# Performance work log

Measured on AMD Instinct MI355X. Metric: run time of the kernel, lower is better.

## Reference

```python
import jax, jax.numpy as jnp
import numpy as np

B, T, C = 4, 4096, 128

def setup_inputs() -> dict:
    key = jax.random.key(0)
    k1, k2, k3, k4 = jax.random.split(key, 4)
    x = jax.random.normal(k1, (B, T, C), dtype=jnp.float32)
    s = 1.0 / np.sqrt(C)
    Wq = jax.random.normal(k2, (C, C), dtype=jnp.float32) * s
    Wk = jax.random.normal(k3, (C, C), dtype=jnp.float32) * s
    Wv = jax.random.normal(k4, (C, C), dtype=jnp.float32) * s
    return {"x": x, "Wq": Wq, "Wk": Wk, "Wv": Wv}

def reference(x, Wq, Wk, Wv):
    # nn.Linear(bias=False): y = x @ W.T
    q = jnp.einsum('btc,dc->btd', x, Wq)
    k = jnp.einsum('btc,dc->btd', x, Wk)
    v = jnp.einsum('btc,dc->btd', x, Wv)
    scale = 1.0 / jnp.sqrt(jnp.asarray(x.shape[-1], x.dtype))
    att = jnp.einsum('btd,bsd->bts', q, k) * scale  # [B,T,T]
    causal = jnp.tril(jnp.ones((x.shape[1], x.shape[1]), dtype=bool))
    att = jnp.where(causal[None, :, :], att, -jnp.inf)
    w = jax.nn.softmax(att, axis=-1)
    # dropout p=0.0 -> identity
    out = jnp.einsum('bts,bsd->btd', w, v)
    return out
```

## Files before the change

kernel.cpp:

```cpp
#include <hip/hip_runtime.h>
#include <hip/hip_bf16.h>
#include <math.h>

#define T_SEQ 4096
#define C_DIM 128
#define B_SZ  4

typedef __attribute__((ext_vector_type(8))) short short8;
typedef __attribute__((ext_vector_type(4))) short short4v;
typedef __attribute__((ext_vector_type(4))) float f32x4;

__device__ __forceinline__ short f2bf(float f) {
    union { float fv; unsigned u; } v; v.fv = f;
    unsigned r = v.u + 0x7fff + ((v.u >> 16) & 1);
    return (short)(r >> 16);
}

__device__ __forceinline__ unsigned pk_bf16(float a, float b) {
    union { __hip_bfloat162 h2; unsigned u; } c;
    c.h2 = __float22bfloat162_rn(make_float2(a, b));
    return c.u;
}

__device__ __forceinline__ short8 load_f32x8_bf16(const float* p) {
    const float4* q = (const float4*)p;
    float4 a = q[0], b = q[1];
    short8 r;
    r[0] = f2bf(a.x); r[1] = f2bf(a.y); r[2] = f2bf(a.z); r[3] = f2bf(a.w);
    r[4] = f2bf(b.x); r[5] = f2bf(b.y); r[6] = f2bf(b.z); r[7] = f2bf(b.w);
    return r;
}

__device__ __forceinline__ void async_cp16(const short* g, short* l) {
    __builtin_amdgcn_global_load_lds(
        (const __attribute__((address_space(1))) unsigned int*)g,
        (__attribute__((address_space(3))) unsigned int*)l, 16, 0, 0);
}

__global__ __launch_bounds__(512) void qkv_proj(
    const float* __restrict__ x, const float* __restrict__ Wq,
    const float* __restrict__ Wk, const float* __restrict__ Wv,
    short* __restrict__ Q, short* __restrict__ Kf, short* __restrict__ Vf)
{
    __shared__ short8 Wl[2048];

    const int tid  = threadIdx.x;
    const int lane = tid & 63;
    const int ln15 = lane & 15;
    const int quad = lane >> 4;
    const int mat  = blockIdx.x >> 6;
    const int rt   = (blockIdx.x & 63) * 8 + (tid >> 6);
    const int m0   = rt * 32;

    const float* W = (mat == 0) ? Wq : (mat == 1) ? Wk : Wv;

    for (int i = tid; i < 2048; i += 512) {
        int n = i >> 4, kc = i & 15;
        short8 v = load_f32x8_bf16(W + n * C_DIM + kc * 8);
        Wl[((n >> 4) * 4 + (kc >> 2)) * 64 + (kc & 3) * 16 + (n & 15)] = v;
    }

    short8 afr[2][4];
#pragma unroll
    for (int ms = 0; ms < 2; ++ms) {
        const float* xrow = x + (size_t)(m0 + ms * 16 + ln15) * C_DIM + quad * 8;
#pragma unroll
        for (int ks = 0; ks < 4; ++ks)
            afr[ms][ks] = load_f32x8_bf16(xrow + ks * 32);
    }

    __syncthreads();

    const float scale = (mat == 0) ? (0.08838834764831845f * 1.4426950408889634f)
                                   : 1.0f;
    const int b  = m0 >> 12;
    const int tl = m0 & 4095;

#pragma unroll
    for (int nt = 0; nt < 8; ++nt) {
        f32x4 acc0 = {0.f, 0.f, 0.f, 0.f};
        f32x4 acc1 = {0.f, 0.f, 0.f, 0.f};
#pragma unroll
        for (int ks = 0; ks < 4; ++ks) {
            short8 bfr = Wl[(nt * 4 + ks) * 64 + lane];
            if (mat == 2) {
                acc0 = __builtin_amdgcn_mfma_f32_16x16x32_bf16(afr[0][ks], bfr, acc0, 0, 0, 0);
                acc1 = __builtin_amdgcn_mfma_f32_16x16x32_bf16(afr[1][ks], bfr, acc1, 0, 0, 0);
            } else {
                acc0 = __builtin_amdgcn_mfma_f32_16x16x32_bf16(bfr, afr[0][ks], acc0, 0, 0, 0);
                acc1 = __builtin_amdgcn_mfma_f32_16x16x32_bf16(bfr, afr[1][ks], acc1, 0, 0, 0);
            }
        }
        if (mat == 0) {
            short4v s0, s1;
#pragma unroll
            for (int r = 0; r < 4; ++r) { s0[r] = f2bf(acc0[r] * scale); s1[r] = f2bf(acc1[r] * scale); }
            *(short4v*)&Q[(size_t)(m0 + ln15) * C_DIM + nt * 16 + quad * 4]      = s0;
            *(short4v*)&Q[(size_t)(m0 + 16 + ln15) * C_DIM + nt * 16 + quad * 4] = s1;
        } else if (mat == 1) {
            const int t16 = tl >> 4;
            short4v s0, s1;
#pragma unroll
            for (int r = 0; r < 4; ++r) { s0[r] = f2bf(acc0[r]); s1[r] = f2bf(acc1[r]); }
            size_t base = (((size_t)(b * 256 + t16) * 4 + (nt >> 1)) << 9)
                        + (((nt & 1) * 2 + (quad >> 1)) * 128) + ln15 * 8 + (quad & 1) * 4;
            *(short4v*)&Kf[base]        = s0;
            *(short4v*)&Kf[base + 2048] = s1;
        } else {
            const int kvc = tl >> 5;
            short4v s0, s1;
#pragma unroll
            for (int r = 0; r < 4; ++r) { s0[r] = f2bf(acc0[r]); s1[r] = f2bf(acc1[r]); }
            short* vbase = Vf + (((size_t)(b * 128 + kvc) * 8 + nt) << 9);
            *(short4v*)&vbase[((quad >> 1) * 16 + ln15) * 8 + (quad & 1) * 4]       = s0;
            *(short4v*)&vbase[(((quad >> 1) + 2) * 16 + ln15) * 8 + (quad & 1) * 4] = s1;
        }
    }
}


#define ROUND_BODY(KC, VC, KN, VN, R)                                        \
  {                                                                          \
    const int kv0 = (R) << 6;                                                \
     \
    asm volatile("s_waitcnt vmcnt(0)" ::: "memory");                         \
    __builtin_amdgcn_sched_barrier(0);                                       \
    __builtin_amdgcn_s_barrier();                                            \
    __builtin_amdgcn_sched_barrier(0);                                       \
    if ((R) + 1 <= kmax) {                                                   \
      const short* gk = Kb + ((size_t)((R) + 1) << 13) + w * 1024;           \
      const short* gv = Vb + ((size_t)((R) + 1) << 13) + w * 1024;           \
      _Pragma("unroll")                                                      \
      for (int i = 0; i < 2; ++i) {                                          \
        async_cp16(gk + i * 512 + lane * 8, &KN[w * 1024 + i * 512]);        \
        async_cp16(gv + i * 512 + lane * 8, &VN[w * 1024 + i * 512]);        \
      }                                                                      \
    }                                                                        \
     \
    short8 kfr[4];                                                           \
    _Pragma("unroll")                                                        \
    for (int ks = 0; ks < 4; ++ks)                                           \
      kfr[ks] = *(const short8*)&KC[(wg * 4 + ks) * 512 + lane * 8];         \
    f32x4 St = {0.f, 0.f, 0.f, 0.f};                                         \
    _Pragma("unroll")                                                        \
    for (int ks = 0; ks < 4; ++ks)                                           \
      St = __builtin_amdgcn_mfma_f32_16x16x32_bf16(kfr[ks], qf[ks], St,      \
                                                   0, 0, 0);                 \
    if (kv0 + 64 > q0) {                                                     \
      const int qcol = q0 + ln15;                                            \
      _Pragma("unroll")                                                      \
      for (int rr = 0; rr < 4; ++rr)                                         \
        if (kv0 + wg * 16 + quad * 4 + rr > qcol) St[rr] = -INFINITY;        \
    }                                                                        \
    {                                                                        \
      float p0 = __builtin_amdgcn_exp2f(St[0] - 16.f);                       \
      float p1 = __builtin_amdgcn_exp2f(St[1] - 16.f);                       \
      float p2 = __builtin_amdgcn_exp2f(St[2] - 16.f);                       \
      float p3 = __builtin_amdgcn_exp2f(St[3] - 16.f);                       \
      l_i += (p0 + p1) + (p2 + p3);                                          \
      uint2 pk;                                                              \
      pk.x = pk_bf16(p0, p1);                                                \
      pk.y = pk_bf16(p2, p3);                                                \
      *(uint2*)&Plds[g][ln15 * 68 + wg * 16 + quad * 4] = pk;                \
    }                                                                        \
           \
    asm volatile("s_waitcnt lgkmcnt(0)" ::: "memory");                       \
    __builtin_amdgcn_sched_barrier(0);                                       \
    __builtin_amdgcn_s_barrier();                                            \
    __builtin_amdgcn_sched_barrier(0);                                       \
           \
    _Pragma("unroll")                                                        \
    for (int kc = 0; kc < 2; ++kc) {                                         \
      short8 vfr[2];                                                         \
      _Pragma("unroll")                                                      \
      for (int di = 0; di < 2; ++di)                                         \
        vfr[di] =                                                            \
            *(const short8*)&VC[(kc * 8 + wg * 2 + di) * 512 + lane * 8];    \
      short8 pf = *(const short8*)&Plds[g][ln15 * 68 + kc * 32 + quad * 8];  \
      _Pragma("unroll")                                                      \
      for (int di = 0; di < 2; ++di)                                         \
        acc[di] = __builtin_amdgcn_mfma_f32_16x16x32_bf16(                   \
            vfr[di], pf, acc[di], 0, 0, 0);                                  \
    }                                                                        \
  }

__global__ __launch_bounds__(512, 2) void flash_attn(
    const short* __restrict__ Q, const short* __restrict__ Kf,
    const short* __restrict__ Vf, float* __restrict__ out)
{
    __shared__ short Klds0[8192];
    __shared__ short Klds1[8192];
    __shared__ short Vlds0[8192];
    __shared__ short Vlds1[8192];
    __shared__ short Plds[2][1088];
    __shared__ float lsum[2][16];

    const int tid  = threadIdx.x;
    const int w    = tid >> 6;
    const int lane = tid & 63;
    const int ln15 = lane & 15;
    const int quad = lane >> 4;
    const int g    = w >> 2;
    const int wg   = w & 3;
    const int bid  = blockIdx.x;
    const int b    = bid & 3;
    const int jj   = bid >> 2;

    const short* Qb = Q  + (size_t)b * T_SEQ * C_DIM;
    const short* Kb = Kf + ((size_t)b << 19);
    const short* Vb = Vf + ((size_t)b << 19);
    float* outb = out + (size_t)b * T_SEQ * C_DIM;

    for (int half = 0; half < 2; ++half) {
        const int p    = half ? (127 - jj) : jj;
        const int q0   = p * 32 + g * 16;
        const int kmax = (p * 32 + 31) >> 6;

        short8 qf[4];
        {
            const short* qrow = Qb + (size_t)(q0 + ln15) * C_DIM + quad * 8;
#pragma unroll
            for (int ks = 0; ks < 4; ++ks)
                qf[ks] = *(const short8*)(qrow + ks * 32);
        }

        f32x4 acc[2];
#pragma unroll
        for (int di = 0; di < 2; ++di)
            acc[di] = (f32x4){0.f, 0.f, 0.f, 0.f};
        float l_i = 0.f;

        {
            const short* gk = Kb + w * 1024;
            const short* gv = Vb + w * 1024;
#pragma unroll
            for (int i = 0; i < 2; ++i) {
                async_cp16(gk + i * 512 + lane * 8, &Klds0[w * 1024 + i * 512]);
                async_cp16(gv + i * 512 + lane * 8, &Vlds0[w * 1024 + i * 512]);
            }
        }

        int r = 0;
        while (true) {
            ROUND_BODY(Klds0, Vlds0, Klds1, Vlds1, r);
            if (++r > kmax) break;
            ROUND_BODY(Klds1, Vlds1, Klds0, Vlds0, r);
            if (++r > kmax) break;
        }

        __syncthreads();
        if (tid < 32) ((float*)lsum)[tid] = 0.f;
        __syncthreads();
        atomicAdd(&lsum[g][ln15], l_i);
        __syncthreads();

        const float li = 1.0f / lsum[g][ln15];
        float* orow = outb + (size_t)(q0 + ln15) * C_DIM;
#pragma unroll
        for (int di = 0; di < 2; ++di) {
            float4 v = make_float4(acc[di][0] * li, acc[di][1] * li,
                                   acc[di][2] * li, acc[di][3] * li);
            *(float4*)&orow[(wg * 2 + di) * 16 + quad * 4] = v;
        }
        __syncthreads();
    }
}

extern "C" void kernel_launch(void* const* d_in, const int* in_sizes, int n_in,
                              void* d_out, int out_size, void* d_ws, size_t ws_size,
                              hipStream_t stream) {
    const float* x  = (const float*)d_in[0];
    const float* Wq = (const float*)d_in[1];
    const float* Wk = (const float*)d_in[2];
    const float* Wv = (const float*)d_in[3];
    float* out = (float*)d_out;

    const size_t elems = (size_t)B_SZ * T_SEQ * C_DIM;
    short* Q  = (short*)d_ws;
    short* Kf = Q  + elems;
    short* Vf = Kf + elems;

    hipLaunchKernelGGL(qkv_proj, dim3(192), dim3(512), 0, stream,
                       x, Wq, Wk, Wv, Q, Kf, Vf);
    hipLaunchKernelGGL(flash_attn, dim3(256), dim3(512), 0, stream,
                       Q, Kf, Vf, out);
}
```

Baseline: 131.4 us.

## Split KV across waves so P stays in registers, removing mid-round barrier

```diff
diff --git a/kernel.cpp b/kernel.cpp
--- a/kernel.cpp
+++ b/kernel.cpp
@@ -98,14 +98,30 @@
             *(short4v*)&Q[(size_t)(m0 + ln15) * C_DIM + nt * 16 + quad * 4]      = s0;
             *(short4v*)&Q[(size_t)(m0 + 16 + ln15) * C_DIM + nt * 16 + quad * 4] = s1;
         } else if (mat == 1) {
-            const int t16 = tl >> 4;
             short4v s0, s1;
 #pragma unroll
             for (int r = 0; r < 4; ++r) { s0[r] = f2bf(acc0[r]); s1[r] = f2bf(acc1[r]); }
-            size_t base = (((size_t)(b * 256 + t16) * 4 + (nt >> 1)) << 9)
-                        + (((nt & 1) * 2 + (quad >> 1)) * 128) + ln15 * 8 + (quad & 1) * 4;
-            *(short4v*)&Kf[base]        = s0;
-            *(short4v*)&Kf[base + 2048] = s1;
+            const int ks     = nt >> 1;
+            const int quad_k = (nt & 1) * 2 + (quad >> 1);
+            const int j0     = (quad & 1) * 4;
+            {
+                const int A0 = (tl >> 4) & 3;
+                const int rd = tl >> 6;
+                const int kt = (A0 >> 1) * 2 + ((ln15 >> 2) & 1);
+                const int ar = (((A0 & 1) << 1) | ((ln15 >> 3) & 1)) * 4 + (ln15 & 3);
+                size_t a = ((size_t)b << 19) + (size_t)rd * 8192
+                         + (kt * 4 + ks) * 512 + quad_k * 128 + ar * 8 + j0;
+                *(short4v*)&Kf[a] = s0;
+            }
+            {
+                const int A1 = ((tl >> 4) + 1) & 3;
+                const int rd = (tl + 16) >> 6;
+                const int kt = (A1 >> 1) * 2 + ((ln15 >> 2) & 1);
+                const int ar = (((A1 & 1) << 1) | ((ln15 >> 3) & 1)) * 4 + (ln15 & 3);
+                size_t a = ((size_t)b << 19) + (size_t)rd * 8192
+                         + (kt * 4 + ks) * 512 + quad_k * 128 + ar * 8 + j0;
+                *(short4v*)&Kf[a] = s1;
+            }
         } else {
             const int kvc = tl >> 5;
             short4v s0, s1;
@@ -128,63 +144,60 @@
     __builtin_amdgcn_s_barrier();                                            \
     __builtin_amdgcn_sched_barrier(0);                                       \
     if ((R) + 1 <= kmax) {                                                   \
-      const short* gk = Kb + ((size_t)((R) + 1) << 13) + w * 1024;           \
-      const short* gv = Vb + ((size_t)((R) + 1) << 13) + w * 1024;           \
+      const short* gk = Kb + (size_t)((R) + 1) * 8192 + w * 2048;            \
+      const short* gv = Vb + (size_t)((R) + 1) * 8192 + w * 2048;            \
       _Pragma("unroll")                                                      \
-      for (int i = 0; i < 2; ++i) {                                          \
-        async_cp16(gk + i * 512 + lane * 8, &KN[w * 1024 + i * 512]);        \
-        async_cp16(gv + i * 512 + lane * 8, &VN[w * 1024 + i * 512]);        \
+      for (int i = 0; i < 4; ++i) {                                          \
+        async_cp16(gk + i * 512 + lane * 8, &KN[w * 2048 + i * 512]);        \
+        async_cp16(gv + i * 512 + lane * 8, &VN[w * 2048 + i * 512]);        \
       }                                                                      \
     }                                                                        \
+              \
+    f32x4 St0 = {0.f, 0.f, 0.f, 0.f}, St1 = {0.f, 0.f, 0.f, 0.f};            \
+    _Pragma("unroll")                                                        \
+    for (int ks = 0; ks < 4; ++ks) {                                         \
+      short8 k0 = *(const short8*)&KC[((s2 + 0) * 4 + ks) * 512 + lane * 8]; \
+      short8 k1 = *(const short8*)&KC[((s2 + 1) * 4 + ks) * 512 + lane * 8]; \
+      St0 = __builtin_amdgcn_mfma_f32_16x16x32_bf16(k0, qf[ks], St0, 0,0,0); \
+      St1 = __builtin_amdgcn_mfma_f32_16x16x32_bf16(k1, qf[ks], St1, 0,0,0); \
+    }                                                                        \
+    \
+    if (kv0 + s * 32 + 31 > q0w) {                                           \
+      const int qcol = q0w + ln15;                                           \
+      const int kb   = kv0 + s * 32 + quad * 8;                              \
+      _Pragma("unroll")                                                      \
+      for (int rr = 0; rr < 4; ++rr) {                                       \
+        if (kb + rr > qcol)     St0[rr] = -INFINITY;                         \
+        if (kb + 4 + rr > qcol) St1[rr] = -INFINITY;                         \
+      }                                                                      \
+    }                                                                        \
      \
-    short8 kfr[4];                                                           \
+    union { unsigned u[4]; short8 s8; } pa;                                  \
+    {                                                                        \
+      float p0 = __builtin_amdgcn_exp2f(St0[0] - 16.f);                      \
+      float p1 = __builtin_amdgcn_exp2f(St0[1] - 16.f);                      \
+      float p2 = __builtin_amdgcn_exp2f(St0[2] - 16.f);                      \
+      float p3 = __builtin_amdgcn_exp2f(St0[3] - 16.f);                      \
+      float p4 = __builtin_amdgcn_exp2f(St1[0] - 16.f);                      \
+      float p5 = __builtin_amdgcn_exp2f(St1[1] - 16.f);                      \
+      float p6 = __builtin_amdgcn_exp2f(St1[2] - 16.f);                      \
+      float p7 = __builtin_amdgcn_exp2f(St1[3] - 16.f);                      \
+      l_i += ((p0 + p1) + (p2 + p3)) + ((p4 + p5) + (p6 + p7));              \
+      pa.u[0] = pk_bf16(p0, p1);                                             \
+      pa.u[1] = pk_bf16(p2, p3);                                             \
+      pa.u[2] = pk_bf16(p4, p5);                                             \
+      pa.u[3] = pk_bf16(p6, p7);                                             \
+    }                                                                        \
+                           \
     _Pragma("unroll")                                                        \
-    for (int ks = 0; ks < 4; ++ks)                                           \
-      kfr[ks] = *(const short8*)&KC[(wg * 4 + ks) * 512 + lane * 8];         \
-    f32x4 St = {0.f, 0.f, 0.f, 0.f};                                         \
-    _Pragma("unroll")                                                        \
-    for (int ks = 0; ks < 4; ++ks)                                           \
-      St = __builtin_amdgcn_mfma_f32_16x16x32_bf16(kfr[ks], qf[ks], St,      \
-                                                   0, 0, 0);                 \
-    if (kv0 + 64 > q0) {                                                     \
-      const int qcol = q0 + ln15;                                            \
-      _Pragma("unroll")                                                      \
-      for (int rr = 0; rr < 4; ++rr)                                         \
-        if (kv0 + wg * 16 + quad * 4 + rr > qcol) St[rr] = -INFINITY;        \
-    }                                                                        \
-    {                                                                        \
-      float p0 = __builtin_amdgcn_exp2f(St[0] - 16.f);                       \
-      float p1 = __builtin_amdgcn_exp2f(St[1] - 16.f);                       \
-      float p2 = __builtin_amdgcn_exp2f(St[2] - 16.f);                       \
-      float p3 = __builtin_amdgcn_exp2f(St[3] - 16.f);                       \
-      l_i += (p0 + p1) + (p2 + p3);                                          \
-      uint2 pk;                                                              \
-      pk.x = pk_bf16(p0, p1);                                                \
-      pk.y = pk_bf16(p2, p3);                                                \
-      *(uint2*)&Plds[g][ln15 * 68 + wg * 16 + quad * 4] = pk;                \
-    }                                                                        \
-           \
-    asm volatile("s_waitcnt lgkmcnt(0)" ::: "memory");                       \
-    __builtin_amdgcn_sched_barrier(0);                                       \
-    __builtin_amdgcn_s_barrier();                                            \
-    __builtin_amdgcn_sched_barrier(0);                                       \
-           \
-    _Pragma("unroll")                                                        \
-    for (int kc = 0; kc < 2; ++kc) {                                         \
-      short8 vfr[2];                                                         \
-      _Pragma("unroll")                                                      \
-      for (int di = 0; di < 2; ++di)                                         \
-        vfr[di] =                                                            \
-            *(const short8*)&VC[(kc * 8 + wg * 2 + di) * 512 + lane * 8];    \
-      short8 pf = *(const short8*)&Plds[g][ln15 * 68 + kc * 32 + quad * 8];  \
-      _Pragma("unroll")                                                      \
-      for (int di = 0; di < 2; ++di)                                         \
-        acc[di] = __builtin_amdgcn_mfma_f32_16x16x32_bf16(                   \
-            vfr[di], pf, acc[di], 0, 0, 0);                                  \
+    for (int dt = 0; dt < 8; ++dt) {                                         \
+      short8 vfr = *(const short8*)&VC[(s * 8 + dt) * 512 + lane * 8];       \
+      acc[dt] = __builtin_amdgcn_mfma_f32_16x16x32_bf16(pa.s8, vfr,          \
+                                                        acc[dt], 0, 0, 0);   \
     }                                                                        \
   }
 
-__global__ __launch_bounds__(512, 2) void flash_attn(
+__global__ __launch_bounds__(256, 1) void flash_attn(
     const short* __restrict__ Q, const short* __restrict__ Kf,
     const short* __restrict__ Vf, float* __restrict__ out)
 {
@@ -192,51 +205,53 @@
     __shared__ short Klds1[8192];
     __shared__ short Vlds0[8192];
     __shared__ short Vlds1[8192];
-    __shared__ short Plds[2][1088];
-    __shared__ float lsum[2][16];
+    __shared__ f32x4 Albuf[2][2][4][64];
+    __shared__ float lsf[2][16];
 
     const int tid  = threadIdx.x;
     const int w    = tid >> 6;
     const int lane = tid & 63;
     const int ln15 = lane & 15;
     const int quad = lane >> 4;
-    const int g    = w >> 2;
-    const int wg   = w & 3;
+    const int qh   = w >> 1;
+    const int s    = w & 1;
+    const int s2   = s << 1;
     const int bid  = blockIdx.x;
     const int b    = bid & 3;
-    const int jj   = bid >> 2;
-
-    const short* Qb = Q  + (size_t)b * T_SEQ * C_DIM;
+    const int pi   = bid >> 2;
+
+    const short* Qb = Q  + ((size_t)b << 19);
     const short* Kb = Kf + ((size_t)b << 19);
     const short* Vb = Vf + ((size_t)b << 19);
-    float* outb = out + (size_t)b * T_SEQ * C_DIM;
+    float* outb = out + ((size_t)b << 19);
 
     for (int half = 0; half < 2; ++half) {
-        const int p    = half ? (127 - jj) : jj;
-        const int q0   = p * 32 + g * 16;
-        const int kmax = (p * 32 + 31) >> 6;
+        const int c    = half ? (127 - pi) : pi;
+        const int q0   = c * 32;
+        const int q0w  = q0 + qh * 16;
+        const int kmax = (q0 + 31) >> 6;
 
         short8 qf[4];
         {
-            const short* qrow = Qb + (size_t)(q0 + ln15) * C_DIM + quad * 8;
+            const short* qrow = Qb + (size_t)(q0w + ln15) * C_DIM + quad * 8;
 #pragma unroll
             for (int ks = 0; ks < 4; ++ks)
                 qf[ks] = *(const short8*)(qrow + ks * 32);
         }
 
-        f32x4 acc[2];
-#pragma unroll
-        for (int di = 0; di < 2; ++di)
-            acc[di] = (f32x4){0.f, 0.f, 0.f, 0.f};
+        f32x4 acc[8];
+#pragma unroll
+        for (int dt = 0; dt < 8; ++dt)
+            acc[dt] = (f32x4){0.f, 0.f, 0.f, 0.f};
         float l_i = 0.f;
 
         {
-            const short* gk = Kb + w * 1024;
-            const short* gv = Vb + w * 1024;
-#pragma unroll
-            for (int i = 0; i < 2; ++i) {
-                async_cp16(gk + i * 512 + lane * 8, &Klds0[w * 1024 + i * 512]);
-                async_cp16(gv + i * 512 + lane * 8, &Vlds0[w * 1024 + i * 512]);
+            const short* gk = Kb + w * 2048;
+            const short* gv = Vb + w * 2048;
+#pragma unroll
+            for (int i = 0; i < 4; ++i) {
+                async_cp16(gk + i * 512 + lane * 8, &Klds0[w * 2048 + i * 512]);
+                async_cp16(gv + i * 512 + lane * 8, &Vlds0[w * 2048 + i * 512]);
             }
         }
 
@@ -249,18 +264,48 @@
         }
 
         __syncthreads();
-        if (tid < 32) ((float*)lsum)[tid] = 0.f;
+        if (tid < 32) ((float*)lsf)[tid] = 0.f;
         __syncthreads();
-        atomicAdd(&lsum[g][ln15], l_i);
+        atomicAdd(&lsf[qh][ln15], l_i);
+        if (s == 0) {
+#pragma unroll
+            for (int d4 = 0; d4 < 4; ++d4)
+                Albuf[qh][1][d4][lane] = acc[4 + d4];
+        } else {
+#pragma unroll
+            for (int d4 = 0; d4 < 4; ++d4)
+                Albuf[qh][0][d4][lane] = acc[d4];
+        }
         __syncthreads();
 
-        const float li = 1.0f / lsum[g][ln15];
-        float* orow = outb + (size_t)(q0 + ln15) * C_DIM;
-#pragma unroll
-        for (int di = 0; di < 2; ++di) {
-            float4 v = make_float4(acc[di][0] * li, acc[di][1] * li,
-                                   acc[di][2] * li, acc[di][3] * li);
-            *(float4*)&orow[(wg * 2 + di) * 16 + quad * 4] = v;
+        float li[4];
+#pragma unroll
+        for (int reg = 0; reg < 4; ++reg)
+            li[reg] = 1.0f / lsf[qh][quad * 4 + reg];
+
+        const int row0 = q0w + quad * 4;
+        if (s == 0) {
+#pragma unroll
+            for (int d4 = 0; d4 < 4; ++d4) {
+                f32x4 o  = acc[d4];
+                f32x4 pr = Albuf[qh][0][d4][lane];
+                const int col = d4 * 16 + ln15;
+#pragma unroll
+                for (int reg = 0; reg < 4; ++reg)
+                    outb[(size_t)(row0 + reg) * C_DIM + col] =
+                        (o[reg] + pr[reg]) * li[reg];
+            }
+        } else {
+#pragma unroll
+            for (int d4 = 0; d4 < 4; ++d4) {
+                f32x4 o  = acc[4 + d4];
+                f32x4 pr = Albuf[qh][1][d4][lane];
+                const int col = (4 + d4) * 16 + ln15;
+#pragma unroll
+                for (int reg = 0; reg < 4; ++reg)
+                    outb[(size_t)(row0 + reg) * C_DIM + col] =
+                        (o[reg] + pr[reg]) * li[reg];
+            }
         }
         __syncthreads();
     }
@@ -282,6 +327,6 @@
 
     hipLaunchKernelGGL(qkv_proj, dim3(192), dim3(512), 0, stream,
                        x, Wq, Wk, Wv, Q, Kf, Vf);
-    hipLaunchKernelGGL(flash_attn, dim3(256), dim3(512), 0, stream,
+    hipLaunchKernelGGL(flash_attn, dim3(256), dim3(256), 0, stream,
                        Q, Kf, Vf, out);
 }
```

Measured after the change: 138.2 us. 1.05x slower.
